# Optimization experiments

Hardware: AMD Instinct MI355X
Metric: run time of the kernel (lower is better)

## Reference

```python
import jax, jax.numpy as jnp
import numpy as np

B, P, G = 16, 4096, 512          # images, proposals/image, gt boxes/image
NUM_CLASSES = 80
IOU_THRESH = 0.5                  # cfg.MODEL.ROI_HEADS.IOU_THRESHOLDS = [0.5]
BATCH_PER_IMG = 512               # cfg.MODEL.ROI_HEADS.BATCH_SIZE_PER_IMAGE
POS_FRAC = 0.25                   # cfg.MODEL.ROI_HEADS.POSITIVE_FRACTION
NUM_FG = int(BATCH_PER_IMG * POS_FRAC)   # 128
NUM_BG = BATCH_PER_IMG - NUM_FG          # 384
NEG_INF = jnp.float32(-1e9)


def _make_boxes(key, b, n, img_size=1024.0):
    # valid xyxy boxes inside an img_size x img_size image
    p = jax.random.uniform(key, (b, n, 4)) * img_size
    x1 = jnp.minimum(p[..., 0], p[..., 2]); x2 = jnp.maximum(p[..., 0], p[..., 2]) + 1.0
    y1 = jnp.minimum(p[..., 1], p[..., 3]); y2 = jnp.maximum(p[..., 1], p[..., 3]) + 1.0
    return jnp.stack([x1, y1, x2, y2], axis=-1)


def setup_inputs() -> dict:
    key = jax.random.key(0)
    k1, k2, k3, k4 = jax.random.split(key, 4)
    return {
        'proposal_boxes': _make_boxes(k1, B, P),
        'target_boxes': _make_boxes(k2, B, G),
        'gt_classes': jax.random.randint(k3, (B, G), 0, NUM_CLASSES),
        'priorities': jax.random.uniform(k4, (B, P)),  # random sampling keys (replaces tf random subsample)
    }


def _pairwise_iou(t, p):
    # t: [B,G,4] gt boxes, p: [B,P,4] proposals, xyxy -> iou [B,G,P]
    area_t = (t[..., 2] - t[..., 0]) * (t[..., 3] - t[..., 1])   # [B,G]
    area_p = (p[..., 2] - p[..., 0]) * (p[..., 3] - p[..., 1])   # [B,P]
    lt = jnp.maximum(t[:, :, None, :2], p[:, None, :, :2])       # [B,G,P,2]
    rb = jnp.minimum(t[:, :, None, 2:], p[:, None, :, 2:])       # [B,G,P,2]
    wh = jnp.clip(rb - lt, 0.0)
    inter = wh[..., 0] * wh[..., 1]                               # [B,G,P]
    union = area_t[:, :, None] + area_p[:, None, :] - inter
    return jnp.where(inter > 0, inter / jnp.maximum(union, 1e-8), 0.0)


def reference(proposal_boxes, target_boxes, gt_classes, priorities):
    # ---- Matcher: pairwise IoU + argmax over gt (thresholds [0.5], labels [0,1]) ----
    iou = _pairwise_iou(target_boxes, proposal_boxes)       # [B,G,P]
    matched_vals = iou.max(axis=1)                          # [B,P]
    matched_idxs = iou.argmax(axis=1)                       # [B,P]
    fg = matched_vals >= IOU_THRESH                         # label==1
    # gt_classes per proposal: matched class if fg, else background = num_classes
    cls_m = jnp.take_along_axis(gt_classes, matched_idxs, axis=1)
    prop_cls = jnp.where(fg, cls_m, NUM_CLASSES)            # [B,P]
    # ---- subsample_labels: pick up to NUM_FG fg and NUM_BG bg by random priority ----
    fg_sc = jnp.where(fg, priorities, NEG_INF)
    bg_sc = jnp.where(~fg, priorities, NEG_INF)
    fg_v, fg_i = jax.lax.top_k(fg_sc, NUM_FG)               # [B,NUM_FG]
    bg_v, bg_i = jax.lax.top_k(bg_sc, NUM_BG)               # [B,NUM_BG]
    inds = jnp.concatenate([fg_i, bg_i], axis=1)            # [B,S]
    valid = jnp.concatenate([fg_v, bg_v], axis=1) > NEG_INF / 2
    # ---- gather sampled proposals + assigned gt (pad_or_clip: zero invalid slots) ----
    s_boxes = jnp.take_along_axis(proposal_boxes, inds[..., None], axis=1)   # [B,S,4]
    s_midx = jnp.take_along_axis(matched_idxs, inds, axis=1)                  # [B,S]
    s_gt_boxes = jnp.take_along_axis(target_boxes, s_midx[..., None], axis=1) # [B,S,4]
    s_cls = jnp.where(valid, jnp.take_along_axis(prop_cls, inds, axis=1), -1) # [B,S]
    mask = valid[..., None].astype(s_boxes.dtype)
    out = jnp.concatenate([s_boxes, s_gt_boxes], axis=-1) * mask              # [B,S,8]
    return out, s_cls
```

## Files before the change

kernel.cpp:

```cpp
#include <hip/hip_runtime.h>
#include <stdint.h>

#define NB 16
#define NP 4096
#define NG 512
#define NCH 8
#define GC  (NG/NCH)
#define NCLS 80
#define KFG 128
#define KBG 384
#define NS 512
#define OUT_BOX (NB*NS*8)
#define OUT_CLS (NB*NS)
#define NBNP (NB*NP)
#define NBK 256
#define NGRP (2*NBK)
#define RBLK 16
#define CHK (NP/RBLK)

typedef unsigned long long u64;

__global__ __launch_bounds__(256) void k_match(
    const float4* __restrict__ prop,
    const float4* __restrict__ tgt,
    u64* __restrict__ pm,
    float* __restrict__ out)
{
    __shared__ float4 tb[GC];
    __shared__ float  ta[GC];

    const int tid  = threadIdx.x;
    const int bx   = blockIdx.x;
    const int c    = bx & (NCH - 1);
    const int pblk = (bx >> 3) & 15;
    const int b    = bx >> 7;

    const int gid = bx * 256 + tid;
    if (gid < OUT_BOX) out[gid] = 0.0f;
    if (gid < OUT_CLS) out[OUT_BOX + gid] = -1.0f;

    if (tid < GC) {
        float4 t = tgt[b * NG + c * GC + tid];
        tb[tid] = t;
        ta[tid] = __fmul_rn(__fsub_rn(t.z, t.x), __fsub_rn(t.w, t.y));
    }
    __syncthreads();

    const int p = pblk * 256 + tid;
    const float4 pb = prop[b * NP + p];
    const float ap = __fmul_rn(__fsub_rn(pb.z, pb.x), __fsub_rn(pb.w, pb.y));

    float best = -1.0f;
    int   bi   = 0;
    #pragma unroll 4
    for (int g = 0; g < GC; ++g) {
        const float4 t = tb[g];
        const float ltx = fmaxf(t.x, pb.x);
        const float lty = fmaxf(t.y, pb.y);
        const float rbx = fminf(t.z, pb.z);
        const float rby = fminf(t.w, pb.w);
        const float w = fmaxf(__fsub_rn(rbx, ltx), 0.0f);
        const float h = fmaxf(__fsub_rn(rby, lty), 0.0f);
        const float inter = __fmul_rn(w, h);
        const float uni   = __fsub_rn(__fadd_rn(ta[g], ap), inter);
        const float tt = __fmul_rn(best, uni);
        const float ss = fmaf(tt, -0x1p-23f, tt);
        if (inter > ss) {
            const float iou = (inter > 0.0f)
                                ? __fdiv_rn(inter, fmaxf(uni, 1e-8f))
                                : 0.0f;
            if (iou > best) { best = iou; bi = g; }
        }
    }
    const int gg = c * GC + bi;
    pm[c * NBNP + b * NP + p] =
        ((u64)__float_as_uint(best) << 16) | (u64)(NG - 1 - gg);
}

__global__ __launch_bounds__(512) void k_rank(
    const float4* __restrict__ prop,
    const float4* __restrict__ tgt,
    const int*   __restrict__ gtc,
    const float* __restrict__ pri,
    const u64*   __restrict__ pm,
    float* __restrict__ out)
{
    __shared__ u64 gkeys[NP];
    __shared__ int cnt[NGRP];
    __shared__ int bsa[NGRP];
    __shared__ int cur[NGRP];
    __shared__ int sA[NGRP], sB[NGRP];
    __shared__ int s_tot0;

    const int tid = threadIdx.x;
    const int b   = blockIdx.x >> 4;
    const int j   = blockIdx.x & (RBLK - 1);

    cnt[tid] = 0;
    __syncthreads();

    u64 skey[8]; short sgrp[8];
    #pragma unroll
    for (int t = 0; t < 8; ++t) {
        const int p = tid + t * 512;
        const int idx = b * NP + p;
        u64 m = pm[idx];
        #pragma unroll
        for (int c = 1; c < NCH; ++c) {
            const u64 mc = pm[c * NBNP + idx];
            if (mc > m) m = mc;
        }
        const float best = __uint_as_float((unsigned)(m >> 16));
        const int cat = (best >= 0.5f) ? 1 : 0;
        const float v = pri[idx];
        int bkt = (int)(v * 256.0f); if (bkt > 255) bkt = 255;
        const int grp = cat * NBK + bkt;
        skey[t] = ((u64)__float_as_uint(v) << 12) | (u64)(NP - 1 - p);
        sgrp[t] = (short)grp;
        atomicAdd(&cnt[grp], 1);
    }
    __syncthreads();

    sA[tid] = cnt[(tid & 256) | (255 - (tid & 255))];
    __syncthreads();

    int* pa = sA; int* pb2 = sB;
    for (int d = 1; d < NGRP; d <<= 1) {
        pb2[tid] = pa[tid] + ((tid >= d) ? pa[tid - d] : 0);
        __syncthreads();
        int* tmp = pa; pa = pb2; pb2 = tmp;
    }
    if (tid == 0) s_tot0 = pa[NBK - 1];
    {
        const int grp = (tid & 256) | (255 - (tid & 255));
        const int excl = pa[tid] - cnt[grp];
        bsa[grp] = excl;
        cur[grp] = excl;
    }
    __syncthreads();

    #pragma unroll
    for (int t = 0; t < 8; ++t) {
        const int off = atomicAdd(&cur[(int)sgrp[t]], 1);
        gkeys[off] = skey[t];
    }
    __syncthreads();

    if (tid < CHK) {
        const int p   = j * CHK + tid;
        const int idx = b * NP + p;
        u64 m = pm[idx];
        #pragma unroll
        for (int c = 1; c < NCH; ++c) {
            const u64 mc = pm[c * NBNP + idx];
            if (mc > m) m = mc;
        }
        const float best = __uint_as_float((unsigned)(m >> 16));
        const int   mi   = (NG - 1) - (int)(m & 0xFFFF);
        const int   cat  = (best >= 0.5f) ? 1 : 0;
        const float v    = pri[idx];
        int bkt = (int)(v * 256.0f); if (bkt > 255) bkt = 255;
        const int grp = cat * NBK + bkt;
        const u64 mine = ((u64)__float_as_uint(v) << 12) | (u64)(NP - 1 - p);

        const int gs = bsa[grp];
        const int gc = cnt[grp];
        int ahead = 0;
        for (int i = gs; i < gs + gc; ++i)
            ahead += (gkeys[i] > mine) ? 1 : 0;
        const int rank = (gs - (cat ? s_tot0 : 0)) + ahead;
        const int cap  = cat ? KFG : KBG;
        if (rank < cap) {
            const int slot = b * NS + (cat ? rank : KFG + rank);
            const float4 pb4 = prop[idx];
            const float4 tb4 = tgt[b * NG + mi];
            float4* orow = (float4*)(out + (size_t)slot * 8);
            orow[0] = pb4;
            orow[1] = tb4;
            out[OUT_BOX + slot] = cat ? (float)gtc[b * NG + mi] : (float)NCLS;
        }
    }
}

extern "C" void kernel_launch(void* const* d_in, const int* in_sizes, int n_in,
                              void* d_out, int out_size, void* d_ws, size_t ws_size,
                              hipStream_t stream) {
    const float4* prop = (const float4*)d_in[0];
    const float4* tgt  = (const float4*)d_in[1];
    const int*    gtc  = (const int*)  d_in[2];
    const float*  pri  = (const float*)d_in[3];
    float* out = (float*)d_out;

    u64* pm = (u64*)d_ws;

    k_match<<<NB * 16 * NCH, 256, 0, stream>>>(prop, tgt, pm, out);
    k_rank<<<NB * RBLK, 512, 0, stream>>>(prop, tgt, gtc, pri, pm, out);
}
```

Measured before the change: 46.88 us.

## Add combine kernel, drop LDS gt staging, and prune ranking to surviving buckets

The match kernel now reads gt boxes straight from global memory and recomputes their areas in the loop, in place of staging them in shared memory. It also drops the early-out test that skipped the divide. A new k_combine kernel reduces the per-chunk matches once per proposal and packs priority, category, bucket and match index into one word. This removes the redundant 8-way reduction that all 16 rank blocks of each image used to repeat. The rank kernel then scatters keys only for buckets that can still fall under the fg/bg caps and skips ranking for proposals in hopeless buckets, at the cost of an extra launch and a workspace round trip.

Measured after the change: 45.38 us. 1.03x faster.

```diff
diff --git a/kernel.cpp b/kernel.cpp
--- a/kernel.cpp
+++ b/kernel.cpp
@@ -26,9 +26,6 @@
     u64* __restrict__ pm,
     float* __restrict__ out)
 {
-    __shared__ float4 tb[GC];
-    __shared__ float  ta[GC];
-
     const int tid  = threadIdx.x;
     const int bx   = blockIdx.x;
     const int c    = bx & (NCH - 1);
@@ -39,22 +36,18 @@
     if (gid < OUT_BOX) out[gid] = 0.0f;
     if (gid < OUT_CLS) out[OUT_BOX + gid] = -1.0f;
 
-    if (tid < GC) {
-        float4 t = tgt[b * NG + c * GC + tid];
-        tb[tid] = t;
-        ta[tid] = __fmul_rn(__fsub_rn(t.z, t.x), __fsub_rn(t.w, t.y));
-    }
-    __syncthreads();
-
     const int p = pblk * 256 + tid;
     const float4 pb = prop[b * NP + p];
     const float ap = __fmul_rn(__fsub_rn(pb.z, pb.x), __fsub_rn(pb.w, pb.y));
 
+    const float4* __restrict__ tg = tgt + b * NG + c * GC;
+
     float best = -1.0f;
     int   bi   = 0;
-    #pragma unroll 4
+    #pragma unroll 8
     for (int g = 0; g < GC; ++g) {
-        const float4 t = tb[g];
+        const float4 t = tg[g];
+        const float at  = __fmul_rn(__fsub_rn(t.z, t.x), __fsub_rn(t.w, t.y));
         const float ltx = fmaxf(t.x, pb.x);
         const float lty = fmaxf(t.y, pb.y);
         const float rbx = fminf(t.z, pb.z);
@@ -62,19 +55,34 @@
         const float w = fmaxf(__fsub_rn(rbx, ltx), 0.0f);
         const float h = fmaxf(__fsub_rn(rby, lty), 0.0f);
         const float inter = __fmul_rn(w, h);
-        const float uni   = __fsub_rn(__fadd_rn(ta[g], ap), inter);
-        const float tt = __fmul_rn(best, uni);
-        const float ss = fmaf(tt, -0x1p-23f, tt);
-        if (inter > ss) {
-            const float iou = (inter > 0.0f)
-                                ? __fdiv_rn(inter, fmaxf(uni, 1e-8f))
-                                : 0.0f;
-            if (iou > best) { best = iou; bi = g; }
-        }
+        const float uni   = __fsub_rn(__fadd_rn(at, ap), inter);
+        const float iou   = __fdiv_rn(inter, fmaxf(uni, 1e-8f));
+        if (iou > best) { best = iou; bi = g; }
     }
     const int gg = c * GC + bi;
     pm[c * NBNP + b * NP + p] =
         ((u64)__float_as_uint(best) << 16) | (u64)(NG - 1 - gg);
+}
+
+__global__ __launch_bounds__(256) void k_combine(
+    const float* __restrict__ pri,
+    const u64*  __restrict__ pm,
+    u64* __restrict__ pmc)
+{
+    const int idx = blockIdx.x * 256 + threadIdx.x;
+    u64 m = pm[idx];
+    #pragma unroll
+    for (int c = 1; c < NCH; ++c) {
+        const u64 mc = pm[c * NBNP + idx];
+        if (mc > m) m = mc;
+    }
+    const float best = __uint_as_float((unsigned)(m >> 16));
+    const int   mi   = (NG - 1) - (int)(m & 0xFFFF);
+    const int   cat  = (best >= 0.5f) ? 1 : 0;
+    const float v    = pri[idx];
+    int bkt = (int)(v * 256.0f); if (bkt > 255) bkt = 255;
+    pmc[idx] = ((u64)__float_as_uint(v) << 18) | ((u64)cat << 17)
+             | ((u64)bkt << 9) | (u64)mi;
 }
 
 __global__ __launch_bounds__(512) void k_rank(
@@ -82,10 +90,11 @@
     const float4* __restrict__ tgt,
     const int*   __restrict__ gtc,
     const float* __restrict__ pri,
-    const u64*   __restrict__ pm,
+    const u64*   __restrict__ pmc,
     float* __restrict__ out)
 {
     __shared__ u64 gkeys[NP];
+    __shared__ unsigned smeta[NP];
     __shared__ int cnt[NGRP];
     __shared__ int bsa[NGRP];
     __shared__ int cur[NGRP];
@@ -99,25 +108,14 @@
     cnt[tid] = 0;
     __syncthreads();
 
-    u64 skey[8]; short sgrp[8];
+    u64 scmb[8];
     #pragma unroll
     for (int t = 0; t < 8; ++t) {
         const int p = tid + t * 512;
-        const int idx = b * NP + p;
-        u64 m = pm[idx];
-        #pragma unroll
-        for (int c = 1; c < NCH; ++c) {
-            const u64 mc = pm[c * NBNP + idx];
-            if (mc > m) m = mc;
-        }
-        const float best = __uint_as_float((unsigned)(m >> 16));
-        const int cat = (best >= 0.5f) ? 1 : 0;
-        const float v = pri[idx];
-        int bkt = (int)(v * 256.0f); if (bkt > 255) bkt = 255;
-        const int grp = cat * NBK + bkt;
-        skey[t] = ((u64)__float_as_uint(v) << 12) | (u64)(NP - 1 - p);
-        sgrp[t] = (short)grp;
-        atomicAdd(&cnt[grp], 1);
+        const u64 cmb = pmc[b * NP + p];
+        scmb[t] = cmb;
+        smeta[p] = (unsigned)(cmb & 0x3FFFFu);
+        atomicAdd(&cnt[(int)((cmb >> 9) & 0x1FF)], 1);
     }
     __syncthreads();
 
@@ -139,45 +137,52 @@
     }
     __syncthreads();
 
+    const int tot0 = s_tot0;
+
     #pragma unroll
     for (int t = 0; t < 8; ++t) {
-        const int off = atomicAdd(&cur[(int)sgrp[t]], 1);
-        gkeys[off] = skey[t];
+        const u64 cmb = scmb[t];
+        const int grp = (int)((cmb >> 9) & 0x1FF);
+        const int cat = (int)((cmb >> 17) & 1);
+        const int gs  = bsa[grp];
+        const int cap = cat ? KFG : KBG;
+        if (gs - (cat ? tot0 : 0) < cap) {
+            const int p = tid + t * 512;
+            const u64 key = ((cmb >> 18) << 12) | (u64)(NP - 1 - p);
+            const int off = atomicAdd(&cur[grp], 1);
+            gkeys[off] = key;
+        }
     }
     __syncthreads();
 
     if (tid < CHK) {
         const int p   = j * CHK + tid;
         const int idx = b * NP + p;
-        u64 m = pm[idx];
-        #pragma unroll
-        for (int c = 1; c < NCH; ++c) {
-            const u64 mc = pm[c * NBNP + idx];
-            if (mc > m) m = mc;
-        }
-        const float best = __uint_as_float((unsigned)(m >> 16));
-        const int   mi   = (NG - 1) - (int)(m & 0xFFFF);
-        const int   cat  = (best >= 0.5f) ? 1 : 0;
-        const float v    = pri[idx];
-        int bkt = (int)(v * 256.0f); if (bkt > 255) bkt = 255;
-        const int grp = cat * NBK + bkt;
-        const u64 mine = ((u64)__float_as_uint(v) << 12) | (u64)(NP - 1 - p);
-
-        const int gs = bsa[grp];
-        const int gc = cnt[grp];
-        int ahead = 0;
-        for (int i = gs; i < gs + gc; ++i)
-            ahead += (gkeys[i] > mine) ? 1 : 0;
-        const int rank = (gs - (cat ? s_tot0 : 0)) + ahead;
-        const int cap  = cat ? KFG : KBG;
-        if (rank < cap) {
-            const int slot = b * NS + (cat ? rank : KFG + rank);
-            const float4 pb4 = prop[idx];
-            const float4 tb4 = tgt[b * NG + mi];
-            float4* orow = (float4*)(out + (size_t)slot * 8);
-            orow[0] = pb4;
-            orow[1] = tb4;
-            out[OUT_BOX + slot] = cat ? (float)gtc[b * NG + mi] : (float)NCLS;
+        const unsigned meta = smeta[p];
+        const int mi  = (int)(meta & 0x1FF);
+        const int cat = (int)((meta >> 17) & 1);
+        const int grp = (int)((meta >> 9) & 0x1FF);
+        const int gs  = bsa[grp];
+        const int catbase = cat ? tot0 : 0;
+        const int cap = cat ? KFG : KBG;
+        if (gs - catbase < cap) {
+            const u64 mine = ((u64)__float_as_uint(pri[idx]) << 12)
+                           | (u64)(NP - 1 - p);
+            const int gc = cnt[grp];
+            int ahead = 0;
+            for (int i = gs; i < gs + gc; ++i)
+                ahead += (gkeys[i] > mine) ? 1 : 0;
+            const int rank = (gs - catbase) + ahead;
+            if (rank < cap) {
+                const int slot = b * NS + (cat ? rank : KFG + rank);
+                const float4 pb4 = prop[idx];
+                const float4 tb4 = tgt[b * NG + mi];
+                float4* orow = (float4*)(out + (size_t)slot * 8);
+                orow[0] = pb4;
+                orow[1] = tb4;
+                out[OUT_BOX + slot] = cat ? (float)gtc[b * NG + mi]
+                                          : (float)NCLS;
+            }
         }
     }
 }
@@ -191,8 +196,10 @@
     const float*  pri  = (const float*)d_in[3];
     float* out = (float*)d_out;
 
-    u64* pm = (u64*)d_ws;
+    u64* pm  = (u64*)d_ws;
+    u64* pmc = (u64*)((char*)d_ws + (size_t)NCH * NBNP * 8);
 
     k_match<<<NB * 16 * NCH, 256, 0, stream>>>(prop, tgt, pm, out);
-    k_rank<<<NB * RBLK, 512, 0, stream>>>(prop, tgt, gtc, pri, pm, out);
-}
+    k_combine<<<NBNP / 256, 256, 0, stream>>>(pri, pm, pmc);
+    k_rank<<<NB * RBLK, 512, 0, stream>>>(prop, tgt, gtc, pri, pmc, out);
+}
```
